# Performance work log

Hardware: AMD Instinct MI355X
Metric: run time of the kernel (lower is better)

The kernel has to match this reference:

```python
import jax, jax.numpy as jnp
import numpy as np

N_NODES = 50000
N_EDGES = 800000
IN_DIM = 128
OUT_DIM = 128


def setup_inputs() -> dict:
    key = jax.random.key(0)
    k1, k2, k3, k4, k5 = jax.random.split(key, 5)
    x = jax.random.normal(k1, (N_NODES, IN_DIM), dtype=jnp.float32)
    # Xavier-uniform-ish scale for the two weight matrices
    scale = float(np.sqrt(6.0 / (IN_DIM + OUT_DIM)))
    Wg = jax.random.uniform(k2, (OUT_DIM, IN_DIM), dtype=jnp.float32, minval=-scale, maxval=scale)
    Wl = jax.random.uniform(k3, (OUT_DIM, IN_DIM), dtype=jnp.float32, minval=-scale, maxval=scale)
    bias = jnp.zeros((OUT_DIM,), dtype=jnp.float32)
    neigh_idx = jax.random.randint(k4, (N_EDGES,), 0, N_NODES, dtype=jnp.int32)
    seg_ids = jnp.sort(jax.random.randint(k5, (N_EDGES,), 0, N_NODES, dtype=jnp.int32))
    return {"x": x, "Wg": Wg, "Wl": Wl, "bias": bias,
            "neigh_idx": neigh_idx, "seg_ids": seg_ids}


def reference(x, Wg, Wl, bias, neigh_idx, seg_ids):
    N = x.shape[0]
    # global 1x1 map on all nodes (self path)
    global_maps = x @ Wg.T                                  # [N, out]
    # per-edge neighbor features: local + global maps of the neighbor
    neigh_x = x[neigh_idx]                                  # [E, in]
    mixed = neigh_x @ Wl.T + global_maps[neigh_idx]         # [E, out]
    # segment-mean over each destination node's neighbors
    sums = jax.ops.segment_sum(mixed, seg_ids, num_segments=N)            # [N, out]
    cnt = jax.ops.segment_sum(jnp.ones((seg_ids.shape[0],), x.dtype), seg_ids, num_segments=N)  # [N]
    mean = sums / jnp.maximum(cnt, 1.0)[:, None]
    # deg == 0 nodes: neigh_agg falls back to global_maps (as in the torch loop)
    neigh_agg = jnp.where((cnt > 0)[:, None], mean, global_maps)
    out = neigh_agg + global_maps + bias
    return jax.nn.elu(out)
```

## Files before the change

kernel.cpp:

```cpp
#include <hip/hip_runtime.h>
#include <hip/hip_bf16.h>

#define NN 50000
#define NE 800000
#define DIM 128
#define NTILES (NN / 16)
#define GEMM_BLOCKS 784

typedef float f32x4 __attribute__((ext_vector_type(4)));
typedef __bf16 bf16x8 __attribute__((ext_vector_type(8)));

static __device__ __forceinline__ float bflo(unsigned v) {
    unsigned b = v << 16; return __builtin_bit_cast(float, b);
}
static __device__ __forceinline__ float bfhi(unsigned v) {
    unsigned b = v & 0xffff0000u; return __builtin_bit_cast(float, b);
}
static __device__ __forceinline__ unsigned short bfbits(float f) {
    __bf16 b = (__bf16)f; return __builtin_bit_cast(unsigned short, b);
}

__global__ void build_v(const float* __restrict__ Wg, const float* __restrict__ Wl,
                        __bf16* __restrict__ V) {
    int i = blockIdx.x * blockDim.x + threadIdx.x;
    if (i >= DIM * 256) return;
    int d = i >> 8;
    int k = i & 255;
    float v;
    if (k < DIM) v = Wg[d * DIM + k];
    else         v = Wg[d * DIM + (k - DIM)] + Wl[d * DIM + (k - DIM)];
    V[i] = (__bf16)v;
}

__global__ void xb_conv(const float* __restrict__ x, __bf16* __restrict__ xb) {
    int i = blockIdx.x * blockDim.x + threadIdx.x;
    const float* p = x + i * 8;
    f32x4 v0 = *reinterpret_cast<const f32x4*>(p);
    f32x4 v1 = *reinterpret_cast<const f32x4*>(p + 4);
    bf16x8 o;
    o[0]=(__bf16)v0[0]; o[1]=(__bf16)v0[1]; o[2]=(__bf16)v0[2]; o[3]=(__bf16)v0[3];
    o[4]=(__bf16)v1[0]; o[5]=(__bf16)v1[1]; o[6]=(__bf16)v1[2]; o[7]=(__bf16)v1[3];
    *reinterpret_cast<bf16x8*>(xb + i * 8) = o;
}

__global__ void build_off(const int* __restrict__ seg, int* __restrict__ off) {
    int n = blockIdx.x * blockDim.x + threadIdx.x;
    if (n > NN) return;
    int lo = 0, hi = NE;
    while (lo < hi) {
        int mid = (lo + hi) >> 1;
        if (seg[mid] < n) lo = mid + 1; else hi = mid;
    }
    off[n] = lo;
}

__global__ void __launch_bounds__(256) seg_mean(const __bf16* __restrict__ xb,
        const int* __restrict__ nidx, const int* __restrict__ off,
        int* __restrict__ cnt_ws, __bf16* __restrict__ meanb) {
    int n = blockIdx.x * 4 + (threadIdx.x >> 6);
    if (n >= NN) return;
    int lane = threadIdx.x & 63;
    int s = off[n], e = off[n + 1];
    const unsigned* xu = reinterpret_cast<const unsigned*>(xb);
    float s0 = 0.f, s1 = 0.f;
    int i = s;
    for (; i + 4 <= e; i += 4) {
        int i0 = nidx[i], i1 = nidx[i+1], i2 = nidx[i+2], i3 = nidx[i+3];
        unsigned v0 = xu[i0 * 64 + lane];
        unsigned v1 = xu[i1 * 64 + lane];
        unsigned v2 = xu[i2 * 64 + lane];
        unsigned v3 = xu[i3 * 64 + lane];
        s0 += bflo(v0) + bflo(v1) + bflo(v2) + bflo(v3);
        s1 += bfhi(v0) + bfhi(v1) + bfhi(v2) + bfhi(v3);
    }
    for (; i < e; ++i) {
        unsigned v = xu[nidx[i] * 64 + lane];
        s0 += bflo(v);
        s1 += bfhi(v);
    }
    int c = e - s;
    float inv = c > 0 ? 1.f / (float)c : 0.f;
    unsigned o = (unsigned)bfbits(s0 * inv) | ((unsigned)bfbits(s1 * inv) << 16);
    reinterpret_cast<unsigned*>(meanb)[n * 64 + lane] = o;
    if (lane == 0) cnt_ws[n] = c;
}

__global__ void __launch_bounds__(256) gemm_ep(const __bf16* __restrict__ xb,
        const __bf16* __restrict__ meanb, const __bf16* __restrict__ V,
        const float* __restrict__ bias, const int* __restrict__ cnt_ws,
        float* __restrict__ out) {
    int tid = threadIdx.x;
    int w = tid >> 6;
    int lane = tid & 63;
    int rowin = lane & 15;
    int kg = lane >> 4;
    int rbase = kg * 4;

    bf16x8 Bf[8][2];
    #pragma unroll
    for (int s = 0; s < 8; ++s)
        #pragma unroll
        for (int ff = 0; ff < 2; ++ff) {
            int d = (w * 2 + ff) * 16 + rowin;
            Bf[s][ff] = *reinterpret_cast<const bf16x8*>(&V[d * 256 + s * 32 + kg * 8]);
        }
    float bs0 = bias[(w * 2) * 16 + rowin];
    float bs1 = bias[(w * 2 + 1) * 16 + rowin];

    for (int t = blockIdx.x; t < NTILES; t += gridDim.x) {
        int m0 = t * 16;
        int row = m0 + rowin;
        f32x4 acc0 = {}, acc1 = {};
        #pragma unroll
        for (int s = 0; s < 4; ++s) {
            bf16x8 a = *reinterpret_cast<const bf16x8*>(&xb[row * DIM + s * 32 + kg * 8]);
            acc0 = __builtin_amdgcn_mfma_f32_16x16x32_bf16(a, Bf[s][0], acc0, 0, 0, 0);
            acc1 = __builtin_amdgcn_mfma_f32_16x16x32_bf16(a, Bf[s][1], acc1, 0, 0, 0);
        }
        #pragma unroll
        for (int s = 0; s < 4; ++s) {
            bf16x8 a = *reinterpret_cast<const bf16x8*>(&meanb[row * DIM + s * 32 + kg * 8]);
            acc0 = __builtin_amdgcn_mfma_f32_16x16x32_bf16(a, Bf[s + 4][0], acc0, 0, 0, 0);
            acc1 = __builtin_amdgcn_mfma_f32_16x16x32_bf16(a, Bf[s + 4][1], acc1, 0, 0, 0);
        }
        #pragma unroll
        for (int r = 0; r < 4; ++r) {
            int n = m0 + rbase + r;
            int c = cnt_ws[n];
            float v0 = acc0[r];
            float z0 = v0 + (c == 0 ? v0 : 0.f) + bs0;
            out[n * DIM + (w * 2) * 16 + rowin] = z0 > 0.f ? z0 : expm1f(z0);
            float v1 = acc1[r];
            float z1 = v1 + (c == 0 ? v1 : 0.f) + bs1;
            out[n * DIM + (w * 2 + 1) * 16 + rowin] = z1 > 0.f ? z1 : expm1f(z1);
        }
    }
}

extern "C" void kernel_launch(void* const* d_in, const int* in_sizes, int n_in,
                              void* d_out, int out_size, void* d_ws, size_t ws_size,
                              hipStream_t stream) {
    const float* x    = (const float*)d_in[0];
    const float* Wg   = (const float*)d_in[1];
    const float* Wl   = (const float*)d_in[2];
    const float* bias = (const float*)d_in[3];
    const int*   nidx = (const int*)d_in[4];
    const int*   seg  = (const int*)d_in[5];
    float* out = (float*)d_out;

    char* p = (char*)d_ws;
    __bf16* V = (__bf16*)p;       p += DIM * 256 * 2;
    int* off = (int*)p;           p += (((NN + 1) * 4) + 511) & ~511ull;
    int* cnt = (int*)p;           p += ((NN * 4) + 511) & ~511ull;
    __bf16* meanb = (__bf16*)p;   p += (size_t)NN * DIM * 2;
    __bf16* xb = (__bf16*)p;

    build_v  <<<(DIM * 256 + 255) / 256, 256, 0, stream>>>(Wg, Wl, V);
    xb_conv  <<<(NN * DIM / 8) / 256, 256, 0, stream>>>(x, xb);
    build_off<<<(NN + 1 + 255) / 256, 256, 0, stream>>>(seg, off);
    seg_mean <<<(NN + 3) / 4, 256, 0, stream>>>(xb, nidx, off, cnt, meanb);
    gemm_ep  <<<GEMM_BLOCKS, 256, 0, stream>>>(xb, meanb, V, bias, cnt, out);
}
```

Before: 155.7 us.

## Fuse segment-mean gather into GEMM epilogue kernel via LDS staging

Merges the separate segment-mean kernel and the persistent GEMM kernel into one kernel per 16-node tile. Each wave gathers neighbor rows with 16-byte loads, four edges in parallel across lane groups, reduces them with cross-lane shuffles, and writes the bf16 mean into LDS, where the MFMA stage reads it. This removes the global round trip of the mean and count buffers and one launch. The cost is reloading the weight fragments into registers in every one of the 3125 blocks, and gather latency that is now exposed inside the GEMM kernel.

```diff
diff --git a/kernel.cpp b/kernel.cpp
--- a/kernel.cpp
+++ b/kernel.cpp
@@ -4,21 +4,10 @@
 #define NN 50000
 #define NE 800000
 #define DIM 128
-#define NTILES (NN / 16)
-#define GEMM_BLOCKS 784
+#define NT (NN / 16)
 
 typedef float f32x4 __attribute__((ext_vector_type(4)));
 typedef __bf16 bf16x8 __attribute__((ext_vector_type(8)));
-
-static __device__ __forceinline__ float bflo(unsigned v) {
-    unsigned b = v << 16; return __builtin_bit_cast(float, b);
-}
-static __device__ __forceinline__ float bfhi(unsigned v) {
-    unsigned b = v & 0xffff0000u; return __builtin_bit_cast(float, b);
-}
-static __device__ __forceinline__ unsigned short bfbits(float f) {
-    __bf16 b = (__bf16)f; return __builtin_bit_cast(unsigned short, b);
-}
 
 __global__ void build_v(const float* __restrict__ Wg, const float* __restrict__ Wl,
                         __bf16* __restrict__ V) {
@@ -54,47 +43,22 @@
     off[n] = lo;
 }
 
-__global__ void __launch_bounds__(256) seg_mean(const __bf16* __restrict__ xb,
+__global__ void __launch_bounds__(256) fused(const __bf16* __restrict__ xb,
+        const __bf16* __restrict__ V, const float* __restrict__ bias,
         const int* __restrict__ nidx, const int* __restrict__ off,
-        int* __restrict__ cnt_ws, __bf16* __restrict__ meanb) {
-    int n = blockIdx.x * 4 + (threadIdx.x >> 6);
-    if (n >= NN) return;
-    int lane = threadIdx.x & 63;
-    int s = off[n], e = off[n + 1];
-    const unsigned* xu = reinterpret_cast<const unsigned*>(xb);
-    float s0 = 0.f, s1 = 0.f;
-    int i = s;
-    for (; i + 4 <= e; i += 4) {
-        int i0 = nidx[i], i1 = nidx[i+1], i2 = nidx[i+2], i3 = nidx[i+3];
-        unsigned v0 = xu[i0 * 64 + lane];
-        unsigned v1 = xu[i1 * 64 + lane];
-        unsigned v2 = xu[i2 * 64 + lane];
-        unsigned v3 = xu[i3 * 64 + lane];
-        s0 += bflo(v0) + bflo(v1) + bflo(v2) + bflo(v3);
-        s1 += bfhi(v0) + bfhi(v1) + bfhi(v2) + bfhi(v3);
-    }
-    for (; i < e; ++i) {
-        unsigned v = xu[nidx[i] * 64 + lane];
-        s0 += bflo(v);
-        s1 += bfhi(v);
-    }
-    int c = e - s;
-    float inv = c > 0 ? 1.f / (float)c : 0.f;
-    unsigned o = (unsigned)bfbits(s0 * inv) | ((unsigned)bfbits(s1 * inv) << 16);
-    reinterpret_cast<unsigned*>(meanb)[n * 64 + lane] = o;
-    if (lane == 0) cnt_ws[n] = c;
-}
+        float* __restrict__ out) {
+    __shared__ __bf16 mean_lds[16 * 136];
+    __shared__ int off_lds[17];
+    __shared__ int cnt_lds[16];
 
-__global__ void __launch_bounds__(256) gemm_ep(const __bf16* __restrict__ xb,
-        const __bf16* __restrict__ meanb, const __bf16* __restrict__ V,
-        const float* __restrict__ bias, const int* __restrict__ cnt_ws,
-        float* __restrict__ out) {
     int tid = threadIdx.x;
     int w = tid >> 6;
     int lane = tid & 63;
     int rowin = lane & 15;
     int kg = lane >> 4;
-    int rbase = kg * 4;
+    int m0 = blockIdx.x * 16;
+
+    if (tid < 17) off_lds[tid] = off[m0 + tid];
 
     bf16x8 Bf[8][2];
     #pragma unroll
@@ -107,33 +71,78 @@
     float bs0 = bias[(w * 2) * 16 + rowin];
     float bs1 = bias[(w * 2 + 1) * 16 + rowin];
 
-    for (int t = blockIdx.x; t < NTILES; t += gridDim.x) {
-        int m0 = t * 16;
+    bf16x8 axs[4];
+    {
         int row = m0 + rowin;
-        f32x4 acc0 = {}, acc1 = {};
         #pragma unroll
-        for (int s = 0; s < 4; ++s) {
-            bf16x8 a = *reinterpret_cast<const bf16x8*>(&xb[row * DIM + s * 32 + kg * 8]);
-            acc0 = __builtin_amdgcn_mfma_f32_16x16x32_bf16(a, Bf[s][0], acc0, 0, 0, 0);
-            acc1 = __builtin_amdgcn_mfma_f32_16x16x32_bf16(a, Bf[s][1], acc1, 0, 0, 0);
+        for (int s = 0; s < 4; ++s)
+            axs[s] = *reinterpret_cast<const bf16x8*>(&xb[row * DIM + s * 32 + kg * 8]);
+    }
+
+    __syncthreads();
+
+    int c0, c1, c2, c3;
+    #pragma unroll
+    for (int j = 0; j < 4; ++j) {
+        int r = w * 4 + j;
+        int s = off_lds[r], e = off_lds[r + 1];
+        float acc[8] = {};
+        #pragma unroll 2
+        for (int i = s; i < e; i += 4) {
+            int ei = i + kg;
+            if (ei < e) {
+                int ni = nidx[ei];
+                bf16x8 v = *reinterpret_cast<const bf16x8*>(&xb[ni * DIM + rowin * 8]);
+                #pragma unroll
+                for (int q = 0; q < 8; ++q) acc[q] += (float)v[q];
+            }
         }
         #pragma unroll
-        for (int s = 0; s < 4; ++s) {
-            bf16x8 a = *reinterpret_cast<const bf16x8*>(&meanb[row * DIM + s * 32 + kg * 8]);
-            acc0 = __builtin_amdgcn_mfma_f32_16x16x32_bf16(a, Bf[s + 4][0], acc0, 0, 0, 0);
-            acc1 = __builtin_amdgcn_mfma_f32_16x16x32_bf16(a, Bf[s + 4][1], acc1, 0, 0, 0);
+        for (int q = 0; q < 8; ++q) {
+            acc[q] += __shfl_xor(acc[q], 16);
+            acc[q] += __shfl_xor(acc[q], 32);
         }
-        #pragma unroll
-        for (int r = 0; r < 4; ++r) {
-            int n = m0 + rbase + r;
-            int c = cnt_ws[n];
-            float v0 = acc0[r];
-            float z0 = v0 + (c == 0 ? v0 : 0.f) + bs0;
-            out[n * DIM + (w * 2) * 16 + rowin] = z0 > 0.f ? z0 : expm1f(z0);
-            float v1 = acc1[r];
-            float z1 = v1 + (c == 0 ? v1 : 0.f) + bs1;
-            out[n * DIM + (w * 2 + 1) * 16 + rowin] = z1 > 0.f ? z1 : expm1f(z1);
+        int c = e - s;
+        if (kg == 0) {
+            float inv = c > 0 ? 1.f / (float)c : 0.f;
+            bf16x8 mv;
+            #pragma unroll
+            for (int q = 0; q < 8; ++q) mv[q] = (__bf16)(acc[q] * inv);
+            *reinterpret_cast<bf16x8*>(&mean_lds[r * 136 + rowin * 8]) = mv;
         }
+        if (j == 0) c0 = c; else if (j == 1) c1 = c; else if (j == 2) c2 = c; else c3 = c;
+    }
+    if (lane == 0) {
+        cnt_lds[w * 4 + 0] = c0; cnt_lds[w * 4 + 1] = c1;
+        cnt_lds[w * 4 + 2] = c2; cnt_lds[w * 4 + 3] = c3;
+    }
+    __syncthreads();
+
+    f32x4 acc0 = {}, acc1 = {};
+    #pragma unroll
+    for (int s = 0; s < 4; ++s) {
+        acc0 = __builtin_amdgcn_mfma_f32_16x16x32_bf16(axs[s], Bf[s][0], acc0, 0, 0, 0);
+        acc1 = __builtin_amdgcn_mfma_f32_16x16x32_bf16(axs[s], Bf[s][1], acc1, 0, 0, 0);
+    }
+    #pragma unroll
+    for (int s = 0; s < 4; ++s) {
+        bf16x8 a = *reinterpret_cast<const bf16x8*>(&mean_lds[rowin * 136 + s * 32 + kg * 8]);
+        acc0 = __builtin_amdgcn_mfma_f32_16x16x32_bf16(a, Bf[s + 4][0], acc0, 0, 0, 0);
+        acc1 = __builtin_amdgcn_mfma_f32_16x16x32_bf16(a, Bf[s + 4][1], acc1, 0, 0, 0);
+    }
+
+    int rbase = kg * 4;
+    #pragma unroll
+    for (int r = 0; r < 4; ++r) {
+        int rr = rbase + r;
+        int n = m0 + rr;
+        int c = cnt_lds[rr];
+        float v0 = acc0[r];
+        float z0 = v0 + (c == 0 ? v0 : 0.f) + bs0;
+        out[n * DIM + (w * 2) * 16 + rowin] = z0 > 0.f ? z0 : expm1f(z0);
+        float v1 = acc1[r];
+        float z1 = v1 + (c == 0 ? v1 : 0.f) + bs1;
+        out[n * DIM + (w * 2 + 1) * 16 + rowin] = z1 > 0.f ? z1 : expm1f(z1);
     }
 }
 
@@ -149,15 +158,12 @@
     float* out = (float*)d_out;
 
     char* p = (char*)d_ws;
-    __bf16* V = (__bf16*)p;       p += DIM * 256 * 2;
-    int* off = (int*)p;           p += (((NN + 1) * 4) + 511) & ~511ull;
-    int* cnt = (int*)p;           p += ((NN * 4) + 511) & ~511ull;
-    __bf16* meanb = (__bf16*)p;   p += (size_t)NN * DIM * 2;
+    __bf16* V = (__bf16*)p;   p += DIM * 256 * 2;
+    int* off = (int*)p;       p += (((NN + 1) * 4) + 511) & ~511ull;
     __bf16* xb = (__bf16*)p;
 
     build_v  <<<(DIM * 256 + 255) / 256, 256, 0, stream>>>(Wg, Wl, V);
     xb_conv  <<<(NN * DIM / 8) / 256, 256, 0, stream>>>(x, xb);
     build_off<<<(NN + 1 + 255) / 256, 256, 0, stream>>>(seg, off);
-    seg_mean <<<(NN + 3) / 4, 256, 0, stream>>>(xb, nidx, off, cnt, meanb);
-    gemm_ep  <<<GEMM_BLOCKS, 256, 0, stream>>>(xb, meanb, V, bias, cnt, out);
+    fused    <<<NT, 256, 0, stream>>>(xb, V, bias, nidx, off, out);
 }
```

Measured after the change: 190.6 us. 1.22x slower.
